# Optimization experiments

Hardware: AMD Instinct MI355X
Metric: run time of the kernel (lower is better)

The kernel has to match this reference:

```python
import jax, jax.numpy as jnp
import numpy as np

B, D, H = 1024, 1024, 4096  # batch, input_dim, hidden_dim
EPS = 1e-3  # keras LayerNormalization default epsilon


def layer_norm(x, gamma, beta):
    m = jnp.mean(x, axis=-1, keepdims=True)
    v = jnp.var(x, axis=-1, keepdims=True)
    return (x - m) * jax.lax.rsqrt(v + EPS) * gamma + beta


def setup_inputs() -> dict:
    key = jax.random.key(0)
    ks = jax.random.split(key, 8)
    C = D + H  # concat width for gate/FFN projections
    s_in = 0.02
    return {
        "x": jax.random.normal(ks[0], (B, D), jnp.float32),
        "hidden_state": jax.random.normal(ks[1], (B, H), jnp.float32),
        "W_u": jax.random.normal(ks[2], (C, H), jnp.float32) * s_in,
        "b_u": jnp.zeros((H,), jnp.float32),
        "W_r": jax.random.normal(ks[3], (C, H), jnp.float32) * s_in,
        "b_r": jnp.zeros((H,), jnp.float32),
        "W_g": jax.random.normal(ks[4], (C, H), jnp.float32) * s_in,
        "b_g": jnp.zeros((H,), jnp.float32),
        "W_up": jax.random.normal(ks[5], (C, H), jnp.float32) * s_in,
        "b_up": jnp.zeros((H,), jnp.float32),
        "W_d": jax.random.normal(ks[6], (H, D), jnp.float32) * s_in,
        "b_d": jnp.zeros((D,), jnp.float32),
        "gamma_h": jnp.ones((H,), jnp.float32),
        "beta_h": jnp.zeros((H,), jnp.float32),
        "gamma_o": jnp.ones((D,), jnp.float32),
        "beta_o": jnp.zeros((D,), jnp.float32),
    }


def reference(x, hidden_state, W_u, b_u, W_r, b_r, W_g, b_g, W_up, b_up,
              W_d, b_d, gamma_h, beta_h, gamma_o, beta_o):
    h = hidden_state
    combined = jnp.concatenate([x, h], axis=-1)          # [B, D+H]
    u = jax.nn.sigmoid(combined @ W_u + b_u)             # update gate [B, H]
    r = jax.nn.sigmoid(combined @ W_r + b_r)             # reset gate  [B, H]
    cand = jnp.concatenate([x, r * h], axis=-1)          # [B, D+H]
    gate = cand @ W_g + b_g
    up = cand @ W_up + b_up
    swiglu = jax.nn.silu(gate) * up                      # [B, H]
    new_h = layer_norm((1.0 - u) * h + u * swiglu + h, gamma_h, beta_h)
    out = layer_norm(new_h @ W_d + b_d, gamma_o, beta_o)  # [B, D]
    return out, new_h
```

## Files before the change

kernel.cpp:

```cpp
#include <hip/hip_runtime.h>
#include <hip/hip_bf16.h>
#include <math.h>


typedef unsigned short u16;
typedef unsigned int u32;
typedef __attribute__((ext_vector_type(8))) short short8;
typedef __attribute__((ext_vector_type(4))) float floatx4;

#define B_ROWS 1024
#define H_DIM 4096
#define D_DIM 1024
#define LDA_S 72

__device__ __forceinline__ float bf2f(u16 v) {
  u32 u = ((u32)v) << 16;
  return __builtin_bit_cast(float, u);
}
__device__ __forceinline__ u16 f2bf(float f) {
  u32 u = __builtin_bit_cast(u32, f);
  u32 r = (u + 0x7fffu + ((u >> 16) & 1u)) >> 16;
  return (u16)r;
}
__device__ __forceinline__ u32 pkbf(float lo, float hi) {
  return (u32)f2bf(lo) | ((u32)f2bf(hi) << 16);
}

__device__ __forceinline__ void gload_lds16(const u16* g, u16* l) {
  __builtin_amdgcn_global_load_lds(
      (const __attribute__((address_space(1))) void*)g,
      (__attribute__((address_space(3))) void*)l, 16, 0, 0);
}


__launch_bounds__(256)
__global__ void conv_w_k(const float* __restrict__ W0, const float* __restrict__ W1,
                         u16* __restrict__ img, int ldb, int KT, int nbHalf) {
  const int nb = blockIdx.x;
  const int kt = blockIdx.y;
  const float* W = (nb < nbHalf) ? W0 : W1;
  const int nbl = (nb < nbHalf) ? nb : (nb - nbHalf);
  const float* src = W + (size_t)kt * 64 * ldb + (size_t)nbl * 128;
  u16* dst = img + ((size_t)nb * KT + kt) * 8192;
  const int t = threadIdx.x;
  const int n = t & 127;
  const int half = t >> 7;
#pragma unroll
  for (int pass = 0; pass < 4; ++pass) {
    const int kc = half * 4 + pass;
    const float* sp = src + (size_t)(kc * 8) * ldb + n;
    uint4 o;
    o.x = pkbf(sp[0],                 sp[(size_t)ldb]);
    o.y = pkbf(sp[(size_t)2 * ldb],   sp[(size_t)3 * ldb]);
    o.z = pkbf(sp[(size_t)4 * ldb],   sp[(size_t)5 * ldb]);
    o.w = pkbf(sp[(size_t)6 * ldb],   sp[(size_t)7 * ldb]);
    *(uint4*)(dst + (size_t)(kc * 128 + n) * 8) = o;
  }
}

__launch_bounds__(256)
__global__ void conv_xh_k(const float* __restrict__ x, const float* __restrict__ h,
                          u16* __restrict__ imgX, u16* __restrict__ imgH) {
  const int kt = blockIdx.x;
  const int mb = blockIdx.y;
  const float* src;
  u16* dst;
  int lda;
  if (kt < 16) {
    lda = 1024;
    src = x + (size_t)mb * 128 * lda + (size_t)kt * 64;
    dst = imgX + ((size_t)mb * 16 + kt) * 8192;
  } else {
    lda = 4096;
    src = h + (size_t)mb * 128 * lda + (size_t)(kt - 16) * 64;
    dst = imgH + ((size_t)mb * 64 + (kt - 16)) * 8192;
  }
  const int t = threadIdx.x;
  const int j = t & 127;
  const int half = t >> 7;
  const float* sp = src + (size_t)j * lda + half * 32;
#pragma unroll
  for (int pass = 0; pass < 4; ++pass) {
    const int kc = half * 4 + pass;
    const float4 a = *(const float4*)(sp + pass * 8);
    const float4 b = *(const float4*)(sp + pass * 8 + 4);
    uint4 o;
    o.x = pkbf(a.x, a.y);
    o.y = pkbf(a.z, a.w);
    o.z = pkbf(b.x, b.y);
    o.w = pkbf(b.z, b.w);
    *(uint4*)(dst + (size_t)(kc * 128 + j) * 8) = o;
  }
}

template <int MODE>
__launch_bounds__(256)
__global__ void gemm_img(const u16* __restrict__ A0, const u16* __restrict__ A1,
                         const u16* __restrict__ Bimg,
                         const float* __restrict__ bias0, const float* __restrict__ bias1,
                         const float* __restrict__ hglob,
                         float* __restrict__ outF, u16* __restrict__ outB0,
                         u16* __restrict__ outB1) {
  constexpr int KT = (MODE == 3) ? 64 : 80;
  constexpr int KSPLIT = (MODE == 3) ? 64 : 16;
  constexpr int A1T = KT - KSPLIT;

  const int bx = blockIdx.x;
  const int by = blockIdx.y;
  const int n0 = bx * 128;
  const int m0 = by * 128;
  const bool second = (MODE != 3) && (n0 >= 4096);
  const int ncol0 = second ? (n0 - 4096) : n0;

  __shared__ __align__(16) u16 As[8192];
  __shared__ __align__(16) u16 Bs[8192];

  const int t = threadIdx.x;
  const int w = t >> 6;
  const int lane = t & 63;
  const int q = lane >> 4;
  const int i16 = lane & 15;
  const int wm = (w >> 1) * 64;
  const int wn = (w & 1) * 64;

  floatx4 acc[4][4] = {};

  const u16* at = A0 + (size_t)by * KSPLIT * 8192;
  const u16* at1 = A1 + (size_t)by * A1T * 8192;
  const u16* btk = Bimg + (size_t)bx * KT * 8192;

  for (int kt = 0; kt < KT; ++kt) {
#pragma unroll
    for (int i = 0; i < 4; ++i) {
      const int ch = (i * 4 + w) * 512;
      gload_lds16(at + ch + lane * 8, &As[ch]);
      gload_lds16(btk + ch + lane * 8, &Bs[ch]);
    }
    __syncthreads();
#pragma unroll
    for (int s = 0; s < 2; ++s) {
      const int c = s * 4 + q;
      short8 av[4], bv[4];
#pragma unroll
      for (int tm = 0; tm < 4; ++tm)
        av[tm] = *(const short8*)(&As[(size_t)(c * 128 + wm + tm * 16 + i16) * 8]);
#pragma unroll
      for (int tn = 0; tn < 4; ++tn)
        bv[tn] = *(const short8*)(&Bs[(size_t)(c * 128 + wn + tn * 16 + i16) * 8]);
#pragma unroll
      for (int tm = 0; tm < 4; ++tm)
#pragma unroll
        for (int tn = 0; tn < 4; ++tn)
          acc[tm][tn] = __builtin_amdgcn_mfma_f32_16x16x32_bf16(av[tm], bv[tn], acc[tm][tn], 0, 0, 0);
    }
    __syncthreads();
    at = (kt == KSPLIT - 1) ? at1 : (at + 8192);
    btk += 8192;
  }

  const float* __restrict__ biasP = second ? bias1 : bias0;
#pragma unroll
  for (int tm = 0; tm < 4; ++tm) {
#pragma unroll
    for (int tn = 0; tn < 4; ++tn) {
      const int nloc = ncol0 + wn + tn * 16 + i16;
      const float b = biasP[nloc];
      const int mbase = m0 + wm + tm * 16 + q * 4;
#pragma unroll
      for (int r = 0; r < 4; ++r) {
        const int m = mbase + r;
        const float v = acc[tm][tn][r] + b;
        if (MODE == 1) {
          const float sg = 1.f / (1.f + __expf(-v));
          if (!second) {
            outF[(size_t)m * 4096 + nloc] = sg;
          } else {
            const float rh = sg * hglob[(size_t)m * 4096 + nloc];
            const size_t tb = ((size_t)(m >> 7) * 64 + (nloc >> 6)) * 8192;
            outB0[tb + (size_t)((((nloc >> 3) & 7) * 128) + (m & 127)) * 8 + (nloc & 7)] = f2bf(rh);
          }
        } else if (MODE == 2) {
          if (!second) outB0[(size_t)m * 4096 + nloc] = f2bf(v);
          else         outB1[(size_t)m * 4096 + nloc] = f2bf(v);
        } else {
          outF[(size_t)m * 1024 + nloc] = v;
        }
      }
    }
  }
}

template <int MODE>
__launch_bounds__(256)
__global__ void gemm_k(const float* __restrict__ Af0, const float* __restrict__ Af1,
                       const u16* __restrict__ Ab,
                       const float* __restrict__ Bg0, const float* __restrict__ Bg1,
                       const float* __restrict__ bias0, const float* __restrict__ bias1,
                       const float* __restrict__ hglob,
                       float* __restrict__ outF, u16* __restrict__ outB0,
                       u16* __restrict__ outB1) {
  constexpr int K_TOT = (MODE == 3) ? 4096 : 5120;
  constexpr int KT = K_TOT / 64;
  constexpr int LDB = (MODE == 3) ? 1024 : 4096;

  const int n0 = blockIdx.x * 128;
  const int m0 = blockIdx.y * 128;
  const bool second = (MODE != 3) && (n0 >= 4096);
  const float* __restrict__ Bg = second ? Bg1 : Bg0;
  const int ncol0 = second ? (n0 - 4096) : n0;

  __shared__ __align__(16) u16 As[128 * LDA_S];
  __shared__ __align__(16) u16 Bs[64 * 128];

  const int t = threadIdx.x;
  const int w = t >> 6;
  const int lane = t & 63;
  const int q = lane >> 4;
  const int i16 = lane & 15;
  const int wm = (w >> 1) * 64;
  const int wn = (w & 1) * 64;

  floatx4 acc[4][4] = {};

  for (int kt = 0; kt < KT; ++kt) {
    const int k0 = kt * 64;
    const bool a_is_bf16 = (MODE == 2) && (k0 >= 1024);
    if (a_is_bf16) {
      const u16* Ag = Ab;
      const int lda = 4096;
      const int krel = k0 - 1024;
#pragma unroll
      for (int c = 0; c < 4; ++c) {
        const int p = c * 256 + t;
        const int row = p >> 3;
        const int cp = p & 7;
        const uint4 v = *(const uint4*)(Ag + (size_t)(m0 + row) * lda + krel + cp * 8);
        *(uint4*)(&As[row * LDA_S + cp * 8]) = v;
      }
    } else {
      const float* Ag;
      int lda, krel;
      if (MODE == 3)      { Ag = Af0; lda = 4096; krel = k0; }
      else if (k0 < 1024) { Ag = Af0; lda = 1024; krel = k0; }
      else                { Ag = Af1; lda = 4096; krel = k0 - 1024; }
#pragma unroll
      for (int c = 0; c < 8; ++c) {
        const int p = c * 256 + t;
        const int row = p >> 4;
        const int cp = p & 15;
        const float4 v = *(const float4*)(Ag + (size_t)(m0 + row) * lda + krel + cp * 4);
        ushort4 o;
        o.x = f2bf(v.x); o.y = f2bf(v.y); o.z = f2bf(v.z); o.w = f2bf(v.w);
        *(ushort4*)(&As[row * LDA_S + cp * 4]) = o;
      }
    }
#pragma unroll
    for (int cc = 0; cc < 2; ++cc) {
      const int c = 2 * w + cc;
      const float* bp = Bg + (size_t)(k0 + c * 8) * LDB + ncol0;
#pragma unroll
      for (int hn = 0; hn < 2; ++hn) {
        const int n = lane + hn * 64;
        const float* src = bp + n;
        u32 p0 = (u32)f2bf(src[0 * LDB]) | ((u32)f2bf(src[1 * LDB]) << 16);
        u32 p1 = (u32)f2bf(src[2 * LDB]) | ((u32)f2bf(src[3 * LDB]) << 16);
        u32 p2 = (u32)f2bf(src[4 * LDB]) | ((u32)f2bf(src[5 * LDB]) << 16);
        u32 p3 = (u32)f2bf(src[6 * LDB]) | ((u32)f2bf(src[7 * LDB]) << 16);
        *(uint4*)(&Bs[(size_t)(c * 128 + n) * 8]) = make_uint4(p0, p1, p2, p3);
      }
    }
    __syncthreads();
#pragma unroll
    for (int s = 0; s < 2; ++s) {
      short8 av[4], bv[4];
#pragma unroll
      for (int tm = 0; tm < 4; ++tm) {
        const int r = wm + tm * 16 + i16;
        av[tm] = *(const short8*)(&As[r * LDA_S + (s * 4 + q) * 8]);
      }
#pragma unroll
      for (int tn = 0; tn < 4; ++tn) {
        const int n = wn + tn * 16 + i16;
        const int c = s * 4 + q;
        bv[tn] = *(const short8*)(&Bs[(size_t)(c * 128 + n) * 8]);
      }
#pragma unroll
      for (int tm = 0; tm < 4; ++tm)
#pragma unroll
        for (int tn = 0; tn < 4; ++tn)
          acc[tm][tn] = __builtin_amdgcn_mfma_f32_16x16x32_bf16(av[tm], bv[tn], acc[tm][tn], 0, 0, 0);
    }
    __syncthreads();
  }

  const float* __restrict__ biasP = second ? bias1 : bias0;
  constexpr int LDO = (MODE == 3) ? 1024 : 4096;
#pragma unroll
  for (int tm = 0; tm < 4; ++tm) {
#pragma unroll
    for (int tn = 0; tn < 4; ++tn) {
      const int nloc = ncol0 + wn + tn * 16 + i16;
      const float b = biasP[nloc];
      const int mbase = m0 + wm + tm * 16 + q * 4;
#pragma unroll
      for (int r = 0; r < 4; ++r) {
        const int m = mbase + r;
        const float v = acc[tm][tn][r] + b;
        const size_t oidx = (size_t)m * LDO + nloc;
        if (MODE == 1) {
          const float sg = 1.f / (1.f + __expf(-v));
          if (!second) outF[oidx] = sg;
          else         outB0[oidx] = f2bf(sg * hglob[oidx]);
        } else if (MODE == 2) {
          if (!second) outB0[oidx] = f2bf(v);
          else         outB1[oidx] = f2bf(v);
        } else {
          outF[oidx] = v;
        }
      }
    }
  }
}

__launch_bounds__(256)
__global__ void ln_h_k(const float* u_f, const u16* __restrict__ wsg,
                       const u16* __restrict__ wsup, const float* __restrict__ h,
                       const float* __restrict__ gamma, const float* __restrict__ beta,
                       float* out, u16* __restrict__ imgNH) {
  const int row = blockIdx.x, t = threadIdx.x;
  const size_t base = (size_t)row * H_DIM;
  const int i0 = t * 16;
  float tv[16];
  float s = 0.f, s2 = 0.f;
#pragma unroll
  for (int j = 0; j < 16; ++j) {
    const int idx = i0 + j;
    const float u = u_f[base + idx];
    const float g = bf2f(wsg[base + idx]);
    const float up = bf2f(wsup[base + idx]);
    const float hh = h[base + idx];
    const float sw = (g / (1.f + __expf(-g))) * up;
    const float x = (2.f - u) * hh + u * sw;
    tv[j] = x; s += x; s2 += x * x;
  }
#pragma unroll
  for (int off = 32; off; off >>= 1) {
    s += __shfl_down(s, off);
    s2 += __shfl_down(s2, off);
  }
  __shared__ float red[8];
  const int w = t >> 6, lane = t & 63;
  if (lane == 0) { red[w] = s; red[4 + w] = s2; }
  __syncthreads();
  const float S = red[0] + red[1] + red[2] + red[3];
  const float S2 = red[4] + red[5] + red[6] + red[7];
  const float mean = S * (1.f / (float)H_DIM);
  const float var = fmaxf(S2 * (1.f / (float)H_DIM) - mean * mean, 0.f);
  const float rstd = rsqrtf(var + 1e-3f);
#pragma unroll
  for (int cc = 0; cc < 2; ++cc) {
    float o[8];
#pragma unroll
    for (int jj = 0; jj < 8; ++jj) {
      const int idx = i0 + cc * 8 + jj;
      o[jj] = (tv[cc * 8 + jj] - mean) * rstd * gamma[idx] + beta[idx];
      out[base + idx] = o[jj];
    }
    if (imgNH) {
      const int idx8 = i0 + cc * 8;
      uint4 v;
      v.x = pkbf(o[0], o[1]);
      v.y = pkbf(o[2], o[3]);
      v.z = pkbf(o[4], o[5]);
      v.w = pkbf(o[6], o[7]);
      *(uint4*)(&imgNH[((size_t)(row >> 7) * 64 + (idx8 >> 6)) * 8192 +
                       (size_t)((((idx8 >> 3) & 7) * 128) + (row & 127)) * 8]) = v;
    }
  }
}

__launch_bounds__(256)
__global__ void ln_o_k(float* io, const float* __restrict__ gamma,
                       const float* __restrict__ beta) {
  const int row = blockIdx.x, t = threadIdx.x;
  const size_t base = (size_t)row * D_DIM;
  const int i0 = t * 4;
  float tv[4];
  float s = 0.f, s2 = 0.f;
#pragma unroll
  for (int j = 0; j < 4; ++j) {
    const float x = io[base + i0 + j];
    tv[j] = x; s += x; s2 += x * x;
  }
#pragma unroll
  for (int off = 32; off; off >>= 1) {
    s += __shfl_down(s, off);
    s2 += __shfl_down(s2, off);
  }
  __shared__ float red[8];
  const int w = t >> 6, lane = t & 63;
  if (lane == 0) { red[w] = s; red[4 + w] = s2; }
  __syncthreads();
  const float S = red[0] + red[1] + red[2] + red[3];
  const float S2 = red[4] + red[5] + red[6] + red[7];
  const float mean = S * (1.f / (float)D_DIM);
  const float var = fmaxf(S2 * (1.f / (float)D_DIM) - mean * mean, 0.f);
  const float rstd = rsqrtf(var + 1e-3f);
#pragma unroll
  for (int j = 0; j < 4; ++j) {
    const int idx = i0 + j;
    io[base + idx] = (tv[j] - mean) * rstd * gamma[idx] + beta[idx];
  }
}

extern "C" void kernel_launch(void* const* d_in, const int* in_sizes, int n_in,
                              void* d_out, int out_size, void* d_ws, size_t ws_size,
                              hipStream_t stream) {
  (void)in_sizes; (void)n_in; (void)out_size;
  const float* x       = (const float*)d_in[0];
  const float* h       = (const float*)d_in[1];
  const float* W_u     = (const float*)d_in[2];
  const float* b_u     = (const float*)d_in[3];
  const float* W_r     = (const float*)d_in[4];
  const float* b_r     = (const float*)d_in[5];
  const float* W_g     = (const float*)d_in[6];
  const float* b_g     = (const float*)d_in[7];
  const float* W_up    = (const float*)d_in[8];
  const float* b_up    = (const float*)d_in[9];
  const float* W_d     = (const float*)d_in[10];
  const float* b_d     = (const float*)d_in[11];
  const float* gamma_h = (const float*)d_in[12];
  const float* beta_h  = (const float*)d_in[13];
  const float* gamma_o = (const float*)d_in[14];
  const float* beta_o  = (const float*)d_in[15];

  float* out_final = (float*)d_out;
  float* out_newh  = (float*)d_out + (size_t)B_ROWS * D_DIM;
  float* u_buf = out_newh;
  float* o_pre = out_final;

  dim3 blk(256);

  const size_t SZ_W  = (size_t)64 * 80 * 16384;
  const size_t SZ_X  = (size_t)8 * 16 * 16384;
  const size_t SZ_H  = (size_t)8 * 64 * 16384;
  const size_t SZ_RH = SZ_H;
  const size_t SZ_G  = (size_t)B_ROWS * H_DIM * 2;
  const size_t SZ_UP = SZ_G;
  const size_t NEED  = SZ_W + SZ_X + SZ_H + SZ_RH + SZ_G + SZ_UP;

  if (ws_size >= NEED) {
    char* ws = (char*)d_ws;
    u16* imgW  = (u16*)(ws);
    u16* imgX  = (u16*)(ws + SZ_W);
    u16* imgH  = (u16*)(ws + SZ_W + SZ_X);
    u16* imgNH = imgH;
    u16* imgRH = (u16*)(ws + SZ_W + SZ_X + SZ_H);
    u16* ws_g  = (u16*)(ws + SZ_W + SZ_X + SZ_H + SZ_RH);
    u16* ws_up = (u16*)(ws + SZ_W + SZ_X + SZ_H + SZ_RH + SZ_G);

    conv_xh_k<<<dim3(80, 8), blk, 0, stream>>>(x, h, imgX, imgH);
    conv_w_k<<<dim3(64, 80), blk, 0, stream>>>(W_u, W_r, imgW, 4096, 80, 32);
    gemm_img<1><<<dim3(64, 8), blk, 0, stream>>>(imgX, imgH, imgW, b_u, b_r, h,
                                                 u_buf, imgRH, nullptr);
    conv_w_k<<<dim3(64, 80), blk, 0, stream>>>(W_g, W_up, imgW, 4096, 80, 32);
    gemm_img<2><<<dim3(64, 8), blk, 0, stream>>>(imgX, imgRH, imgW, b_g, b_up, nullptr,
                                                 nullptr, ws_g, ws_up);
    ln_h_k<<<dim3(B_ROWS), blk, 0, stream>>>(u_buf, ws_g, ws_up, h, gamma_h, beta_h,
                                             out_newh, imgNH);
    conv_w_k<<<dim3(8, 64), blk, 0, stream>>>(W_d, nullptr, imgW, 1024, 64, 8);
    gemm_img<3><<<dim3(8, 8), blk, 0, stream>>>(imgNH, imgNH, imgW, b_d, nullptr, nullptr,
                                                o_pre, nullptr, nullptr);
    ln_o_k<<<dim3(B_ROWS), blk, 0, stream>>>(o_pre, gamma_o, beta_o);
  } else {
    char* ws = (char*)d_ws;
    u16* ws_rh = (u16*)(ws);
    u16* ws_g  = (u16*)(ws + (size_t)8 * 1024 * 1024);
    u16* ws_up = (u16*)(ws + (size_t)16 * 1024 * 1024);

    gemm_k<1><<<dim3(64, 8), blk, 0, stream>>>(x, h, nullptr, W_u, W_r, b_u, b_r, h,
                                               u_buf, ws_rh, nullptr);
    gemm_k<2><<<dim3(64, 8), blk, 0, stream>>>(x, nullptr, ws_rh, W_g, W_up, b_g, b_up,
                                               nullptr, nullptr, ws_g, ws_up);
    ln_h_k<<<dim3(B_ROWS), blk, 0, stream>>>(u_buf, ws_g, ws_up, h, gamma_h, beta_h,
                                             out_newh, nullptr);
    gemm_k<3><<<dim3(8, 8), blk, 0, stream>>>(out_newh, nullptr, nullptr, W_d, nullptr,
                                              b_d, nullptr, nullptr, o_pre, nullptr, nullptr);
    ln_o_k<<<dim3(B_ROWS), blk, 0, stream>>>(o_pre, gamma_o, beta_o);
  }
}
```

Measured before the change: 699.2 us.

## Split-K the output projection and double-buffer LDS tiles in image GEMM

The final W_d GEMM is split four ways over K using a z grid dimension, writing fp32 partials into reused workspace. The output layernorm kernel now sums the partials and adds the bias before normalising, which fixes the underfilled 64-block launch. All image GEMMs also stage the next K tile into a second LDS buffer while computing on the current one, so loads can overlap MFMA. The cost is extra partial-buffer traffic, doubled LDS use per block, and reliance on async load completion ordering with a single barrier.

```diff
diff --git a/kernel.cpp b/kernel.cpp
--- a/kernel.cpp
+++ b/kernel.cpp
@@ -101,19 +101,20 @@
                          const float* __restrict__ hglob,
                          float* __restrict__ outF, u16* __restrict__ outB0,
                          u16* __restrict__ outB1) {
-  constexpr int KT = (MODE == 3) ? 64 : 80;
-  constexpr int KSPLIT = (MODE == 3) ? 64 : 16;
-  constexpr int A1T = KT - KSPLIT;
+  constexpr int KT = (MODE == 3) ? 16 : 80;
+  constexpr int KSPLIT = 16;
+  constexpr int KT_B = (MODE == 3) ? 64 : 80;
 
   const int bx = blockIdx.x;
   const int by = blockIdx.y;
+  const int kz = (MODE == 3) ? (int)blockIdx.z * 16 : 0;
   const int n0 = bx * 128;
   const int m0 = by * 128;
   const bool second = (MODE != 3) && (n0 >= 4096);
   const int ncol0 = second ? (n0 - 4096) : n0;
 
-  __shared__ __align__(16) u16 As[8192];
-  __shared__ __align__(16) u16 Bs[8192];
+  __shared__ __align__(16) u16 As[2][8192];
+  __shared__ __align__(16) u16 Bs[2][8192];
 
   const int t = threadIdx.x;
   const int w = t >> 6;
@@ -125,28 +126,43 @@
 
   floatx4 acc[4][4] = {};
 
-  const u16* at = A0 + (size_t)by * KSPLIT * 8192;
-  const u16* at1 = A1 + (size_t)by * A1T * 8192;
-  const u16* btk = Bimg + (size_t)bx * KT * 8192;
-
-  for (int kt = 0; kt < KT; ++kt) {
+  const u16* btile = Bimg + ((size_t)bx * KT_B + kz) * 8192;
+
+  auto stage = [&](int kt, int buf) {
+    const u16* a;
+    if (MODE == 3) {
+      a = A0 + ((size_t)by * 64 + kz + kt) * 8192;
+    } else {
+      a = (kt < KSPLIT) ? A0 + ((size_t)by * 16 + kt) * 8192
+                        : A1 + ((size_t)by * 64 + (kt - KSPLIT)) * 8192;
+    }
+    const u16* b = btile + (size_t)kt * 8192;
+    u16* As_ = &As[buf][0];
+    u16* Bs_ = &Bs[buf][0];
 #pragma unroll
     for (int i = 0; i < 4; ++i) {
       const int ch = (i * 4 + w) * 512;
-      gload_lds16(at + ch + lane * 8, &As[ch]);
-      gload_lds16(btk + ch + lane * 8, &Bs[ch]);
-    }
-    __syncthreads();
+      gload_lds16(a + ch + lane * 8, As_ + ch);
+      gload_lds16(b + ch + lane * 8, Bs_ + ch);
+    }
+  };
+
+  stage(0, 0);
+  __syncthreads();
+  int cur = 0;
+
+  for (int kt = 0; kt < KT; ++kt) {
+    if (kt + 1 < KT) stage(kt + 1, cur ^ 1);
 #pragma unroll
     for (int s = 0; s < 2; ++s) {
       const int c = s * 4 + q;
       short8 av[4], bv[4];
 #pragma unroll
       for (int tm = 0; tm < 4; ++tm)
-        av[tm] = *(const short8*)(&As[(size_t)(c * 128 + wm + tm * 16 + i16) * 8]);
+        av[tm] = *(const short8*)(&As[cur][(size_t)(c * 128 + wm + tm * 16 + i16) * 8]);
 #pragma unroll
       for (int tn = 0; tn < 4; ++tn)
-        bv[tn] = *(const short8*)(&Bs[(size_t)(c * 128 + wn + tn * 16 + i16) * 8]);
+        bv[tn] = *(const short8*)(&Bs[cur][(size_t)(c * 128 + wn + tn * 16 + i16) * 8]);
 #pragma unroll
       for (int tm = 0; tm < 4; ++tm)
 #pragma unroll
@@ -154,17 +170,17 @@
           acc[tm][tn] = __builtin_amdgcn_mfma_f32_16x16x32_bf16(av[tm], bv[tn], acc[tm][tn], 0, 0, 0);
     }
     __syncthreads();
-    at = (kt == KSPLIT - 1) ? at1 : (at + 8192);
-    btk += 8192;
+    cur ^= 1;
   }
 
   const float* __restrict__ biasP = second ? bias1 : bias0;
+  float* __restrict__ outP = (MODE == 3) ? outF + (size_t)blockIdx.z * (1024 * 1024) : outF;
 #pragma unroll
   for (int tm = 0; tm < 4; ++tm) {
 #pragma unroll
     for (int tn = 0; tn < 4; ++tn) {
       const int nloc = ncol0 + wn + tn * 16 + i16;
-      const float b = biasP[nloc];
+      const float b = (MODE == 3) ? 0.f : biasP[nloc];
       const int mbase = m0 + wm + tm * 16 + q * 4;
 #pragma unroll
       for (int r = 0; r < 4; ++r) {
@@ -183,7 +199,7 @@
           if (!second) outB0[(size_t)m * 4096 + nloc] = f2bf(v);
           else         outB1[(size_t)m * 4096 + nloc] = f2bf(v);
         } else {
-          outF[(size_t)m * 1024 + nloc] = v;
+          outP[(size_t)m * 1024 + nloc] = v;
         }
       }
     }
@@ -380,8 +396,46 @@
 }
 
 __launch_bounds__(256)
-__global__ void ln_o_k(float* io, const float* __restrict__ gamma,
-                       const float* __restrict__ beta) {
+__global__ void ln_o_k(const float* __restrict__ part, const float* __restrict__ bias,
+                       const float* __restrict__ gamma, const float* __restrict__ beta,
+                       float* __restrict__ out) {
+  const int row = blockIdx.x, t = threadIdx.x;
+  const size_t base = (size_t)row * D_DIM;
+  const int i0 = t * 4;
+  constexpr size_t PSTRIDE = (size_t)1024 * 1024;
+  float tv[4];
+  float s = 0.f, s2 = 0.f;
+#pragma unroll
+  for (int j = 0; j < 4; ++j) {
+    const size_t idx = base + i0 + j;
+    const float x = part[idx] + part[idx + PSTRIDE] + part[idx + 2 * PSTRIDE] +
+                    part[idx + 3 * PSTRIDE] + bias[i0 + j];
+    tv[j] = x; s += x; s2 += x * x;
+  }
+#pragma unroll
+  for (int off = 32; off; off >>= 1) {
+    s += __shfl_down(s, off);
+    s2 += __shfl_down(s2, off);
+  }
+  __shared__ float red[8];
+  const int w = t >> 6, lane = t & 63;
+  if (lane == 0) { red[w] = s; red[4 + w] = s2; }
+  __syncthreads();
+  const float S = red[0] + red[1] + red[2] + red[3];
+  const float S2 = red[4] + red[5] + red[6] + red[7];
+  const float mean = S * (1.f / (float)D_DIM);
+  const float var = fmaxf(S2 * (1.f / (float)D_DIM) - mean * mean, 0.f);
+  const float rstd = rsqrtf(var + 1e-3f);
+#pragma unroll
+  for (int j = 0; j < 4; ++j) {
+    const int idx = i0 + j;
+    out[base + idx] = (tv[j] - mean) * rstd * gamma[idx] + beta[idx];
+  }
+}
+
+__launch_bounds__(256)
+__global__ void ln_o_fb(float* io, const float* __restrict__ gamma,
+                        const float* __restrict__ beta) {
   const int row = blockIdx.x, t = threadIdx.x;
   const size_t base = (size_t)row * D_DIM;
   const int i0 = t * 4;
@@ -458,6 +512,7 @@
     u16* imgRH = (u16*)(ws + SZ_W + SZ_X + SZ_H);
     u16* ws_g  = (u16*)(ws + SZ_W + SZ_X + SZ_H + SZ_RH);
     u16* ws_up = (u16*)(ws + SZ_W + SZ_X + SZ_H + SZ_RH + SZ_G);
+    float* part = (float*)ws_g;
 
     conv_xh_k<<<dim3(80, 8), blk, 0, stream>>>(x, h, imgX, imgH);
     conv_w_k<<<dim3(64, 80), blk, 0, stream>>>(W_u, W_r, imgW, 4096, 80, 32);
@@ -469,9 +524,9 @@
     ln_h_k<<<dim3(B_ROWS), blk, 0, stream>>>(u_buf, ws_g, ws_up, h, gamma_h, beta_h,
                                              out_newh, imgNH);
     conv_w_k<<<dim3(8, 64), blk, 0, stream>>>(W_d, nullptr, imgW, 1024, 64, 8);
-    gemm_img<3><<<dim3(8, 8), blk, 0, stream>>>(imgNH, imgNH, imgW, b_d, nullptr, nullptr,
-                                                o_pre, nullptr, nullptr);
-    ln_o_k<<<dim3(B_ROWS), blk, 0, stream>>>(o_pre, gamma_o, beta_o);
+    gemm_img<3><<<dim3(8, 8, 4), blk, 0, stream>>>(imgNH, imgNH, imgW, nullptr, nullptr,
+                                                   nullptr, part, nullptr, nullptr);
+    ln_o_k<<<dim3(B_ROWS), blk, 0, stream>>>(part, b_d, gamma_o, beta_o, out_final);
   } else {
     char* ws = (char*)d_ws;
     u16* ws_rh = (u16*)(ws);
@@ -486,6 +541,6 @@
                                              out_newh, nullptr);
     gemm_k<3><<<dim3(8, 8), blk, 0, stream>>>(out_newh, nullptr, nullptr, W_d, nullptr,
                                               b_d, nullptr, nullptr, o_pre, nullptr, nullptr);
-    ln_o_k<<<dim3(B_ROWS), blk, 0, stream>>>(o_pre, gamma_o, beta_o);
-  }
-}
+    ln_o_fb<<<dim3(B_ROWS), blk, 0, stream>>>(o_pre, gamma_o, beta_o);
+  }
+}
```

Measured after the change: 643.5 us. 8.0% less time.
